# Performance work log

Hardware: AMD Instinct MI355X
Metric: run time of the kernel (lower is better)

Reference implementation:

```python
import jax, jax.numpy as jnp
import numpy as np

B, T, E, NH = 2, 2048, 512, 8
HD = E // NH
SCALE = float(HD) ** -0.5


def setup_inputs() -> dict:
    key = jax.random.key(0)
    ks = jax.random.split(key, 7)
    s = 0.02
    return {
        "x": jax.random.normal(ks[0], (B, T, E), dtype=jnp.float32),
        "w_qkv": jax.random.normal(ks[1], (E, 3 * E), dtype=jnp.float32) * s,
        "b_qkv": jax.random.normal(ks[2], (3 * E,), dtype=jnp.float32) * s,
        "w_od": jax.random.normal(ks[3], (E, 2 * NH), dtype=jnp.float32) * s,
        "b_od": jax.random.normal(ks[4], (2 * NH,), dtype=jnp.float32) * s,
        "w_out": jax.random.normal(ks[5], (E, E), dtype=jnp.float32) * s,
        "b_out": jax.random.normal(ks[6], (E,), dtype=jnp.float32) * s,
    }


def _heads(t):  # (B,T,E) -> (B*NH, T, HD)
    return t.reshape(B, T, NH, HD).transpose(0, 2, 1, 3).reshape(B * NH, T, HD)


def _point_mask(idx, j):  # idx: (B*NH,T) float indices -> one-hot (B*NH,T,T)
    return (j[None, None, :] == idx[:, :, None]).astype(jnp.float32)


def reference(x, w_qkv, b_qkv, w_od, b_od, w_out, b_out):
    qkv = x @ w_qkv + b_qkv
    Q, K, V = jnp.split(qkv, 3, axis=-1)  # each (B,T,E)

    od = Q @ w_od + b_od  # (B,T,2*NH)
    offset, duration = jnp.split(od, 2, axis=-1)
    offset = jnp.tanh(offset) * T
    duration = jax.nn.sigmoid(duration) * T

    query_index = jnp.arange(T, dtype=x.dtype)[None, :, None]  # (1,T,1)
    anchor = query_index + offset  # (B,T,NH)
    # 'b t nh -> (b nh) t'
    anchor = anchor.transpose(0, 2, 1).reshape(B * NH, T)
    duration = duration.transpose(0, 2, 1).reshape(B * NH, T)

    start = anchor - duration
    end = anchor + duration
    bound_l = jnp.floor(start)
    bound_r = jnp.ceil(end)
    anchor_l = jnp.floor(anchor)
    anchor_r = anchor_l + 1.0

    j = jnp.arange(T, dtype=x.dtype)
    neg_bound_weight = (bound_l - start)[:, :, None] * _point_mask(bound_l, j) \
                     + (end - bound_r)[:, :, None] * _point_mask(bound_r, j)
    anchor_dist_l = anchor - anchor_l
    anchor_weight = anchor_dist_l[:, :, None] * _point_mask(anchor_r, j) \
                  + (1.0 - anchor_dist_l)[:, :, None] * _point_mask(anchor_l, j)
    point_weight = 1.0 + neg_bound_weight + anchor_weight  # (B*NH,T,T)

    # segment mask: True OUTSIDE [bound_l, bound_r]
    attn_mask = (j[None, None, :] < bound_l[:, :, None]) | (j[None, None, :] > bound_r[:, :, None])

    Qh, Kh, Vh = _heads(Q), _heads(K), _heads(V)  # (B*NH, T, HD)
    scores = jnp.einsum('bic,brc->bir', Qh, Kh) * SCALE * point_weight
    scores = jnp.where(attn_mask, jnp.asarray(-1e8, scores.dtype), scores)
    attn = jax.nn.softmax(scores, axis=-1)
    out = jnp.einsum('bir,brc->bic', attn, Vh)  # (B*NH,T,HD)
    out = out.reshape(B, NH, T, HD).transpose(0, 2, 1, 3).reshape(B, T, E)
    return out @ w_out + b_out
```

## Files before the change

### kernel.cpp

```cpp
#include <hip/hip_runtime.h>
#include <math.h>

typedef float vf4 __attribute__((ext_vector_type(4)));
typedef float f32x4 __attribute__((ext_vector_type(4)));
typedef short bf16x8 __attribute__((ext_vector_type(8)));
typedef short short4v __attribute__((ext_vector_type(4)));

constexpr int B = 2, T = 2048, E = 512, NH = 8, HD = 64;
constexpr int BH = B * NH;
constexpr int NT = BH * T;
constexpr float SCALE = 0.125f;

static __device__ __forceinline__ short f2bf(float f) {
  unsigned u = __float_as_uint(f);
  unsigned r = (u + 0x7fffu + ((u >> 16) & 1u)) >> 16;
  return (short)r;
}

__global__ __launch_bounds__(256) void cast_x_bf16(
    const float* __restrict__ x, short* __restrict__ xb)
{
  int idx = (blockIdx.x * 256 + threadIdx.x) * 4;
  vf4 v = *(const vf4*)&x[idx];
  short4v o;
  o[0] = f2bf(v[0]); o[1] = f2bf(v[1]); o[2] = f2bf(v[2]); o[3] = f2bf(v[3]);
  *(short4v*)&xb[idx] = o;
}

__global__ __launch_bounds__(256) void cast_w_T(
    const float* __restrict__ w, short* __restrict__ wT, int N)
{
  __shared__ float t[32][33];
  const int k0 = blockIdx.x * 32;
  const int n0 = blockIdx.y * 32;
  const int c = threadIdx.x & 31, r = threadIdx.x >> 5;
#pragma unroll
  for (int p = 0; p < 4; ++p)
    t[r + p * 8][c] = w[(size_t)(k0 + r + p * 8) * N + n0 + c];
  __syncthreads();
#pragma unroll
  for (int p = 0; p < 4; ++p)
    wT[(size_t)(n0 + r + p * 8) * 512 + k0 + c] = f2bf(t[c][r + p * 8]);
}

__global__ __launch_bounds__(256) void w_comb(
    const float* __restrict__ w_qkv, const float* __restrict__ b_qkv,
    const float* __restrict__ w_od, const float* __restrict__ b_od,
    float* __restrict__ Wc, float* __restrict__ bc)
{
  const int tid = threadIdx.x;
  if (blockIdx.x < 32) {
    const int k = blockIdx.x * 16 + (tid >> 4);
    const int c = tid & 15;
    float s = 0.0f;
    for (int m = 0; m < E; ++m)
      s += w_qkv[(size_t)k * 1536 + m] * w_od[m * 16 + c];
    Wc[k * 16 + c] = s;
  } else if (tid < 16) {
    const int c = tid;
    float s = b_od[c];
    for (int m = 0; m < E; ++m)
      s += b_qkv[m] * w_od[m * 16 + c];
    bc[c] = s;
  }
}

__global__ __launch_bounds__(256) void qkv_gemm_bf16(
    const short* __restrict__ xb, const short* __restrict__ wT,
    const float* __restrict__ bias, short* __restrict__ qkvb)
{
  __shared__ short As[128 * 40];
  __shared__ short Bt[64 * 40];

  const int tid = threadIdx.x;
  const int wave = tid >> 6, lane = tid & 63;
  const int quad = lane >> 4, l15 = lane & 15;
  const int wm = wave >> 1, wn = wave & 1;
  const int m0 = blockIdx.y * 128, n0 = blockIdx.x * 64;

  f32x4 acc[4][2];
#pragma unroll
  for (int mi = 0; mi < 4; ++mi)
#pragma unroll
    for (int ni = 0; ni < 2; ++ni) acc[mi][ni] = (f32x4){0, 0, 0, 0};

  const int ar = tid >> 2, akc = (tid & 3) * 8;
  const int br_ = tid >> 2, bkc = (tid & 3) * 8;

#pragma unroll 1
  for (int k0 = 0; k0 < E; k0 += 32) {
    __syncthreads();
    *(bf16x8*)&As[ar * 40 + akc] =
        *(const bf16x8*)&xb[(size_t)(m0 + ar) * 512 + k0 + akc];
    *(bf16x8*)&As[(64 + ar) * 40 + akc] =
        *(const bf16x8*)&xb[(size_t)(m0 + 64 + ar) * 512 + k0 + akc];
    if (br_ < 64)
      *(bf16x8*)&Bt[br_ * 40 + bkc] =
          *(const bf16x8*)&wT[(size_t)(n0 + br_) * 512 + k0 + bkc];
    __syncthreads();

    bf16x8 aA[4], bB[2];
#pragma unroll
    for (int mi = 0; mi < 4; ++mi)
      aA[mi] = *(const bf16x8*)&As[(wm * 64 + mi * 16 + l15) * 40 + quad * 8];
#pragma unroll
    for (int ni = 0; ni < 2; ++ni)
      bB[ni] = *(const bf16x8*)&Bt[(wn * 32 + ni * 16 + l15) * 40 + quad * 8];
#pragma unroll
    for (int mi = 0; mi < 4; ++mi)
#pragma unroll
      for (int ni = 0; ni < 2; ++ni)
        acc[mi][ni] = __builtin_amdgcn_mfma_f32_16x16x32_bf16(
            aA[mi], bB[ni], acc[mi][ni], 0, 0, 0);
  }

#pragma unroll
  for (int mi = 0; mi < 4; ++mi)
#pragma unroll
    for (int ni = 0; ni < 2; ++ni)
#pragma unroll
      for (int r = 0; r < 4; ++r) {
        int row = m0 + wm * 64 + mi * 16 + quad * 4 + r;
        int col = n0 + wn * 32 + ni * 16 + l15;
        float v = acc[mi][ni][r] + bias[col];
        if (col < 512) v *= SCALE;
        qkvb[(size_t)row * 1536 + col] = f2bf(v);
      }
}

__global__ __launch_bounds__(256) void od_params(
    const float* __restrict__ x, const float* __restrict__ Wc,
    const float* __restrict__ bc, float* __restrict__ prm)
{
  __shared__ float od_s[16][16];
  const int tid = threadIdx.x;
  const int r = tid >> 4, c = tid & 15;
  const int row = blockIdx.x * 16 + r;

  float sum = bc[c];
  const float* qr = x + (size_t)row * E;
  for (int k = 0; k < E; k += 4) {
    vf4 q = *(const vf4*)&qr[k];
    sum += q[0] * Wc[(k + 0) * 16 + c]
         + q[1] * Wc[(k + 1) * 16 + c]
         + q[2] * Wc[(k + 2) * 16 + c]
         + q[3] * Wc[(k + 3) * 16 + c];
  }
  od_s[r][c] = sum;
  __syncthreads();

  if (tid < 128) {
    const int rr = tid >> 3, h = tid & 7;
    const int grow = blockIdx.x * 16 + rr;
    const int b = grow / T, i = grow % T;
    float o = od_s[rr][h];
    float d = od_s[rr][h + 8];
    float offset   = tanhf(o) * (float)T;
    float duration = (float)T / (1.0f + expf(-d));
    float anchor = (float)i + offset;
    float start = anchor - duration;
    float end   = anchor + duration;
    float bl = floorf(start);
    float br = ceilf(end);
    float al = floorf(anchor);
    float wbl = bl - start;
    float wbr = end - br;
    float af  = anchor - al;
    float rsc = 1.0f;
    if (br < 0.0f || bl > (float)(T - 1)) {
      bl = 0.0f; br = (float)(T - 1);
      wbl = 0.0f; wbr = 0.0f; al = -5.0f; af = 0.0f;
      rsc = 0.0f;
    }
    int idx = (b * NH + h) * T + i;
    prm[0 * NT + idx] = bl;
    prm[1 * NT + idx] = br;
    prm[2 * NT + idx] = wbl;
    prm[3 * NT + idx] = wbr;
    prm[4 * NT + idx] = al;
    prm[5 * NT + idx] = af;
    prm[6 * NT + idx] = rsc;
  }
}

__global__ __launch_bounds__(256) void flash_attn_mfma2(
    const short* __restrict__ qkvb, const float* __restrict__ prm,
    float* __restrict__ Opart, float* __restrict__ lpart)
{
  __shared__ short Qs[64 * 72];
  __shared__ short Ks[64 * 72];
  __shared__ short Vt[64 * 72];
  __shared__ short Ps[4][16 * 72];
  __shared__ float u_s[8];

  const int tid = threadIdx.x;
  const int wave = tid >> 6, lane = tid & 63;
  const int quad = lane >> 4, l15 = lane & 15;
  const int qt = blockIdx.x, bh = blockIdx.y, ks = blockIdx.z;
  const int b = bh >> 3, h = bh & 7;
  const int i0 = qt * 64;

  float bl[4], br[4], wbl[4], wbr[4], al[4], af[4], rsc[4];
  {
    int rowp = bh * T + i0 + wave * 16 + quad * 4;
#pragma unroll
    for (int r = 0; r < 4; ++r) {
      bl[r]  = prm[0 * NT + rowp + r];
      br[r]  = prm[1 * NT + rowp + r];
      wbl[r] = prm[2 * NT + rowp + r];
      wbr[r] = prm[3 * NT + rowp + r];
      al[r]  = prm[4 * NT + rowp + r];
      af[r]  = prm[5 * NT + rowp + r];
      rsc[r] = prm[6 * NT + rowp + r];
    }
  }

  float bmn = fminf(fminf(bl[0], bl[1]), fminf(bl[2], bl[3]));
  float bmx = fmaxf(fmaxf(br[0], br[1]), fmaxf(br[2], br[3]));
#pragma unroll
  for (int d = 16; d < 64; d <<= 1) {
    bmn = fminf(bmn, __shfl_xor(bmn, d));
    bmx = fmaxf(bmx, __shfl_xor(bmx, d));
  }
  if (lane == 0) { u_s[wave * 2] = bmn; u_s[wave * 2 + 1] = bmx; }

  {
    const int rq = tid >> 3, cb = (tid & 7) * 8;
#pragma unroll
    for (int it = 0; it < 2; ++it) {
      int rr = it * 32 + rq;
      *(bf16x8*)&Qs[rr * 72 + cb] =
          *(const bf16x8*)&qkvb[(size_t)(b * T + i0 + rr) * 1536 + h * 64 + cb];
    }
  }
  __syncthreads();
  bmn = fminf(fminf(u_s[0], u_s[2]), fminf(u_s[4], u_s[6]));
  bmx = fmaxf(fmaxf(u_s[1], u_s[3]), fmaxf(u_s[5], u_s[7]));
  const int ktlo = max(ks * 16, max(((int)bmn) >> 6, 0));
  const int kthi = min(ks * 16 + 15, min(((int)bmx) >> 6, T / 64 - 1));

  f32x4 o[4];
#pragma unroll
  for (int c = 0; c < 4; ++c) o[c] = (f32x4){0, 0, 0, 0};
  float lacc[4] = {0, 0, 0, 0};

  const int rq = tid >> 3, cb = (tid & 7) * 8;
  const int kw_sw = (cb >> 3) << 3;

#pragma unroll 1
  for (int kt = ktlo; kt <= kthi; ++kt) {
    const int j0 = kt * 64;
    __syncthreads();
#pragma unroll
    for (int it = 0; it < 2; ++it) {
      int rr = it * 32 + rq;
      size_t base = (size_t)(b * T + j0 + rr) * 1536 + h * 64 + cb;
      *(bf16x8*)&Ks[rr * 72 + cb] = *(const bf16x8*)&qkvb[base + 512];
      bf16x8 v = *(const bf16x8*)&qkvb[base + 1024];
      int kw = rr ^ kw_sw;
#pragma unroll
      for (int j = 0; j < 8; ++j) Vt[(cb + j) * 72 + kw] = v[j];
    }
    __syncthreads();

    bf16x8 aQ0 = *(const bf16x8*)&Qs[(wave * 16 + l15) * 72 + quad * 8];
    bf16x8 aQ1 = *(const bf16x8*)&Qs[(wave * 16 + l15) * 72 + 32 + quad * 8];
    f32x4 s[4];
#pragma unroll
    for (int nc = 0; nc < 4; ++nc) {
      const short* kb = &Ks[(nc * 16 + l15) * 72 + quad * 8];
      f32x4 a = (f32x4){0, 0, 0, 0};
      a = __builtin_amdgcn_mfma_f32_16x16x32_bf16(aQ0, *(const bf16x8*)&kb[0],  a, 0, 0, 0);
      a = __builtin_amdgcn_mfma_f32_16x16x32_bf16(aQ1, *(const bf16x8*)&kb[32], a, 0, 0, 0);
      s[nc] = a;
    }

    const float jf0 = (float)(j0 + l15);
#pragma unroll
    for (int nc = 0; nc < 4; ++nc) {
      float jf = jf0 + (float)(nc * 16);
#pragma unroll
      for (int r = 0; r < 4; ++r) {
        float w = 1.0f;
        w += (jf == bl[r]) ? wbl[r] : 0.0f;
        w += (jf == br[r]) ? wbr[r] : 0.0f;
        w += (jf == al[r]) ? (1.0f - af[r]) : 0.0f;
        w += (jf == al[r] + 1.0f) ? af[r] : 0.0f;
        float v = s[nc][r] * w * rsc[r];
        v = (jf < bl[r] || jf > br[r]) ? -30.0f : v;
        float p = __expf(v);
        lacc[r] += p;
        Ps[wave][(quad * 4 + r) * 72 + nc * 16 + l15] = f2bf(p);
      }
    }
    __syncthreads();

    bf16x8 aP0 = *(const bf16x8*)&Ps[wave][l15 * 72 + quad * 8];
    bf16x8 aP1 = *(const bf16x8*)&Ps[wave][l15 * 72 + 32 + quad * 8];
#pragma unroll
    for (int c = 0; c < 4; ++c) {
      int hd = c * 16 + l15;
      int g = (hd >> 3) & 7;
      const short* vb = &Vt[hd * 72];
      int blk0 = (quad) ^ g;
      int blk1 = (4 + quad) ^ g;
      o[c] = __builtin_amdgcn_mfma_f32_16x16x32_bf16(
          aP0, *(const bf16x8*)&vb[blk0 * 8], o[c], 0, 0, 0);
      o[c] = __builtin_amdgcn_mfma_f32_16x16x32_bf16(
          aP1, *(const bf16x8*)&vb[blk1 * 8], o[c], 0, 0, 0);
    }
  }

#pragma unroll
  for (int d = 1; d < 16; d <<= 1)
#pragma unroll
    for (int r = 0; r < 4; ++r)
      lacc[r] += __shfl_xor(lacc[r], d);

  const int rowb = i0 + wave * 16 + quad * 4;
  if (l15 == 0) {
#pragma unroll
    for (int r = 0; r < 4; ++r)
      lpart[ks * NT + bh * T + rowb + r] = lacc[r];
  }
#pragma unroll
  for (int r = 0; r < 4; ++r) {
    size_t base = (size_t)ks * (B * T * E) + (size_t)(b * T + rowb + r) * E + h * 64;
#pragma unroll
    for (int c = 0; c < 4; ++c)
      Opart[base + c * 16 + l15] = o[c][r];
  }
}

__global__ __launch_bounds__(256) void combine_attn(
    const float* __restrict__ Opart, const float* __restrict__ lpart,
    short* __restrict__ attnb)
{
  int base = (blockIdx.x * 256 + threadIdx.x) * 4;
  int row = base >> 9;
  int c = base & 511;
  int h = c >> 6;
  int b = row >> 11;
  int i = row & (T - 1);
  int lidx = ((b << 3) + h) * T + i;
  float l = lpart[lidx] + lpart[NT + lidx];
  float inv = 1.0f / l;
  vf4 o0 = *(const vf4*)&Opart[base];
  vf4 o1 = *(const vf4*)&Opart[(size_t)(B * T * E) + base];
  short4v ov;
#pragma unroll
  for (int j = 0; j < 4; ++j) ov[j] = f2bf((o0[j] + o1[j]) * inv);
  *(short4v*)&attnb[base] = ov;
}

__global__ __launch_bounds__(256) void out_gemm_bf16(
    const short* __restrict__ Ab, const short* __restrict__ wT,
    const float* __restrict__ bias, float* __restrict__ Co)
{
  __shared__ short As[64 * 40];
  __shared__ short Bt[64 * 40];

  const int tid = threadIdx.x;
  const int wave = tid >> 6, lane = tid & 63;
  const int quad = lane >> 4, l15 = lane & 15;
  const int wm = wave >> 1, wn = wave & 1;
  const int m0 = blockIdx.y * 64, n0 = blockIdx.x * 64;

  f32x4 acc[2][2];
#pragma unroll
  for (int mi = 0; mi < 2; ++mi)
#pragma unroll
    for (int ni = 0; ni < 2; ++ni) acc[mi][ni] = (f32x4){0, 0, 0, 0};

  const int ar = tid >> 2, akc = (tid & 3) * 8;

#pragma unroll 1
  for (int k0 = 0; k0 < E; k0 += 32) {
    __syncthreads();
    *(bf16x8*)&As[ar * 40 + akc] =
        *(const bf16x8*)&Ab[(size_t)(m0 + ar) * 512 + k0 + akc];
    *(bf16x8*)&Bt[ar * 40 + akc] =
        *(const bf16x8*)&wT[(size_t)(n0 + ar) * 512 + k0 + akc];
    __syncthreads();

    bf16x8 aA[2], bB[2];
#pragma unroll
    for (int mi = 0; mi < 2; ++mi)
      aA[mi] = *(const bf16x8*)&As[(wm * 32 + mi * 16 + l15) * 40 + quad * 8];
#pragma unroll
    for (int ni = 0; ni < 2; ++ni)
      bB[ni] = *(const bf16x8*)&Bt[(wn * 32 + ni * 16 + l15) * 40 + quad * 8];
#pragma unroll
    for (int mi = 0; mi < 2; ++mi)
#pragma unroll
      for (int ni = 0; ni < 2; ++ni)
        acc[mi][ni] = __builtin_amdgcn_mfma_f32_16x16x32_bf16(
            aA[mi], bB[ni], acc[mi][ni], 0, 0, 0);
  }

#pragma unroll
  for (int mi = 0; mi < 2; ++mi)
#pragma unroll
    for (int ni = 0; ni < 2; ++ni)
#pragma unroll
      for (int r = 0; r < 4; ++r) {
        int row = m0 + wm * 32 + mi * 16 + quad * 4 + r;
        int col = n0 + wn * 32 + ni * 16 + l15;
        Co[(size_t)row * 512 + col] = acc[mi][ni][r] + bias[col];
      }
}

extern "C" void kernel_launch(void* const* d_in, const int* in_sizes, int n_in,
                              void* d_out, int out_size, void* d_ws, size_t ws_size,
                              hipStream_t stream)
{
  const float* x     = (const float*)d_in[0];
  const float* w_qkv = (const float*)d_in[1];
  const float* b_qkv = (const float*)d_in[2];
  const float* w_od  = (const float*)d_in[3];
  const float* b_od  = (const float*)d_in[4];
  const float* w_out = (const float*)d_in[5];
  const float* b_out = (const float*)d_in[6];
  float* out = (float*)d_out;

  char* w = (char*)d_ws;
  short* xb    = (short*)w;  w += (size_t)B * T * E * 2;
  short* wTq   = (short*)w;  w += (size_t)E * 3 * E * 2;
  short* wTo   = (short*)w;  w += (size_t)E * E * 2;
  short* qkvb  = (short*)w;  w += (size_t)B * T * 3 * E * 2;
  float* Wc    = (float*)w;  w += (size_t)E * 16 * 4;
  float* bc    = (float*)w;  w += 256;
  float* prm   = (float*)w;  w += (size_t)7 * NT * 4;
  float* Opart = (float*)w;  w += (size_t)2 * B * T * E * 4;
  float* lpart = (float*)w;  w += (size_t)2 * NT * 4;
  short* attnb = (short*)w;  w += (size_t)B * T * E * 2;

  cast_x_bf16<<<dim3(B * T * E / 1024), 256, 0, stream>>>(x, xb);
  cast_w_T<<<dim3(E / 32, 3 * E / 32), 256, 0, stream>>>(w_qkv, wTq, 3 * E);
  cast_w_T<<<dim3(E / 32, E / 32), 256, 0, stream>>>(w_out, wTo, E);
  w_comb<<<dim3(33), 256, 0, stream>>>(w_qkv, b_qkv, w_od, b_od, Wc, bc);

  qkv_gemm_bf16<<<dim3(3 * E / 64, B * T / 128), 256, 0, stream>>>(
      xb, wTq, b_qkv, qkvb);

  od_params<<<dim3(B * T / 16), 256, 0, stream>>>(x, Wc, bc, prm);

  flash_attn_mfma2<<<dim3(T / 64, BH, 2), 256, 0, stream>>>(
      qkvb, prm, Opart, lpart);

  combine_attn<<<dim3(B * T * E / 1024), 256, 0, stream>>>(Opart, lpart, attnb);

  out_gemm_bf16<<<dim3(E / 64, B * T / 64), 256, 0, stream>>>(
      attnb, wTo, b_out, out);
}
```

Measured before the change: 197.3 us.

## Pretranspose V globally, swap MFMA operands in attention, widen QKV GEMM tile

Adds a separate kernel that transposes V into a head-major layout so the attention loop loads V tiles directly instead of scattering a transpose into shared memory every iteration. The attention kernel keeps Q in registers, swaps the MFMA operand order so each lane owns one query row, and replaces float comparisons for the point and segment weights with integer offset tests. It also writes P with packed stores, drops one barrier, and uses vectorised output stores. Separately, the QKV GEMM tile widens to 128x128, and w_comb stages w_od in shared memory and parallelises the bias reduction. The cost is an extra launch and one pass over V, with the transposed V reusing the xb buffer.

```diff
diff --git a/kernel.cpp b/kernel.cpp
--- a/kernel.cpp
+++ b/kernel.cpp
@@ -5,6 +5,7 @@
 typedef float f32x4 __attribute__((ext_vector_type(4)));
 typedef short bf16x8 __attribute__((ext_vector_type(8)));
 typedef short short4v __attribute__((ext_vector_type(4)));
+typedef int int2v __attribute__((ext_vector_type(2)));
 
 constexpr int B = 2, T = 2048, E = 512, NH = 8, HD = 64;
 constexpr int BH = B * NH;
@@ -15,6 +16,11 @@
   unsigned u = __float_as_uint(f);
   unsigned r = (u + 0x7fffu + ((u >> 16) & 1u)) >> 16;
   return (short)r;
+}
+static __device__ __forceinline__ unsigned pk2bf(float a, float b) {
+  unsigned lo = (unsigned)(unsigned short)f2bf(a);
+  unsigned hi = (unsigned)(unsigned short)f2bf(b);
+  return lo | (hi << 16);
 }
 
 __global__ __launch_bounds__(256) void cast_x_bf16(
@@ -48,20 +54,39 @@
     const float* __restrict__ w_od, const float* __restrict__ b_od,
     float* __restrict__ Wc, float* __restrict__ bc)
 {
-  const int tid = threadIdx.x;
+  __shared__ float Lod[512 * 16];
+  __shared__ float pb[16][17];
+  const int tid = threadIdx.x;
+#pragma unroll
+  for (int p = 0; p < 8; ++p) {
+    int idx = (p * 256 + tid) * 4;
+    *(vf4*)&Lod[idx] = *(const vf4*)&w_od[idx];
+  }
+  __syncthreads();
+
   if (blockIdx.x < 32) {
     const int k = blockIdx.x * 16 + (tid >> 4);
     const int c = tid & 15;
     float s = 0.0f;
-    for (int m = 0; m < E; ++m)
-      s += w_qkv[(size_t)k * 1536 + m] * w_od[m * 16 + c];
+    for (int m = 0; m < E; m += 4) {
+      vf4 wq = *(const vf4*)&w_qkv[(size_t)k * 1536 + m];
+      s += wq[0] * Lod[(m + 0) * 16 + c] + wq[1] * Lod[(m + 1) * 16 + c]
+         + wq[2] * Lod[(m + 2) * 16 + c] + wq[3] * Lod[(m + 3) * 16 + c];
+    }
     Wc[k * 16 + c] = s;
-  } else if (tid < 16) {
-    const int c = tid;
-    float s = b_od[c];
-    for (int m = 0; m < E; ++m)
-      s += b_qkv[m] * w_od[m * 16 + c];
-    bc[c] = s;
+  } else {
+    const int c = tid & 15, seg = tid >> 4;
+    float s = 0.0f;
+    for (int m = seg * 32; m < seg * 32 + 32; ++m)
+      s += b_qkv[m] * Lod[m * 16 + c];
+    pb[seg][c] = s;
+    __syncthreads();
+    if (tid < 16) {
+      float acc = b_od[tid];
+#pragma unroll
+      for (int g = 0; g < 16; ++g) acc += pb[g][tid];
+      bc[tid] = acc;
+    }
   }
 }
 
@@ -69,47 +94,47 @@
     const short* __restrict__ xb, const short* __restrict__ wT,
     const float* __restrict__ bias, short* __restrict__ qkvb)
 {
-  __shared__ short As[128 * 40];
-  __shared__ short Bt[64 * 40];
+  __shared__ __align__(16) short As[128 * 40];
+  __shared__ __align__(16) short Bt[128 * 40];
 
   const int tid = threadIdx.x;
   const int wave = tid >> 6, lane = tid & 63;
   const int quad = lane >> 4, l15 = lane & 15;
   const int wm = wave >> 1, wn = wave & 1;
-  const int m0 = blockIdx.y * 128, n0 = blockIdx.x * 64;
-
-  f32x4 acc[4][2];
+  const int m0 = blockIdx.y * 128, n0 = blockIdx.x * 128;
+
+  f32x4 acc[4][4];
 #pragma unroll
   for (int mi = 0; mi < 4; ++mi)
 #pragma unroll
-    for (int ni = 0; ni < 2; ++ni) acc[mi][ni] = (f32x4){0, 0, 0, 0};
-
-  const int ar = tid >> 2, akc = (tid & 3) * 8;
-  const int br_ = tid >> 2, bkc = (tid & 3) * 8;
+    for (int ni = 0; ni < 4; ++ni) acc[mi][ni] = (f32x4){0, 0, 0, 0};
+
+  const int sr = tid >> 1, sc = (tid & 1) * 16;
 
 #pragma unroll 1
   for (int k0 = 0; k0 < E; k0 += 32) {
     __syncthreads();
-    *(bf16x8*)&As[ar * 40 + akc] =
-        *(const bf16x8*)&xb[(size_t)(m0 + ar) * 512 + k0 + akc];
-    *(bf16x8*)&As[(64 + ar) * 40 + akc] =
-        *(const bf16x8*)&xb[(size_t)(m0 + 64 + ar) * 512 + k0 + akc];
-    if (br_ < 64)
-      *(bf16x8*)&Bt[br_ * 40 + bkc] =
-          *(const bf16x8*)&wT[(size_t)(n0 + br_) * 512 + k0 + bkc];
-    __syncthreads();
-
-    bf16x8 aA[4], bB[2];
+    *(bf16x8*)&As[sr * 40 + sc] =
+        *(const bf16x8*)&xb[(size_t)(m0 + sr) * 512 + k0 + sc];
+    *(bf16x8*)&As[sr * 40 + sc + 8] =
+        *(const bf16x8*)&xb[(size_t)(m0 + sr) * 512 + k0 + sc + 8];
+    *(bf16x8*)&Bt[sr * 40 + sc] =
+        *(const bf16x8*)&wT[(size_t)(n0 + sr) * 512 + k0 + sc];
+    *(bf16x8*)&Bt[sr * 40 + sc + 8] =
+        *(const bf16x8*)&wT[(size_t)(n0 + sr) * 512 + k0 + sc + 8];
+    __syncthreads();
+
+    bf16x8 aA[4], bB[4];
 #pragma unroll
     for (int mi = 0; mi < 4; ++mi)
       aA[mi] = *(const bf16x8*)&As[(wm * 64 + mi * 16 + l15) * 40 + quad * 8];
 #pragma unroll
-    for (int ni = 0; ni < 2; ++ni)
-      bB[ni] = *(const bf16x8*)&Bt[(wn * 32 + ni * 16 + l15) * 40 + quad * 8];
+    for (int ni = 0; ni < 4; ++ni)
+      bB[ni] = *(const bf16x8*)&Bt[(wn * 64 + ni * 16 + l15) * 40 + quad * 8];
 #pragma unroll
     for (int mi = 0; mi < 4; ++mi)
 #pragma unroll
-      for (int ni = 0; ni < 2; ++ni)
+      for (int ni = 0; ni < 4; ++ni)
         acc[mi][ni] = __builtin_amdgcn_mfma_f32_16x16x32_bf16(
             aA[mi], bB[ni], acc[mi][ni], 0, 0, 0);
   }
@@ -117,11 +142,11 @@
 #pragma unroll
   for (int mi = 0; mi < 4; ++mi)
 #pragma unroll
-    for (int ni = 0; ni < 2; ++ni)
+    for (int ni = 0; ni < 4; ++ni)
 #pragma unroll
       for (int r = 0; r < 4; ++r) {
         int row = m0 + wm * 64 + mi * 16 + quad * 4 + r;
-        int col = n0 + wn * 32 + ni * 16 + l15;
+        int col = n0 + wn * 64 + ni * 16 + l15;
         float v = acc[mi][ni][r] + bias[col];
         if (col < 512) v *= SCALE;
         qkvb[(size_t)row * 1536 + col] = f2bf(v);
@@ -183,14 +208,37 @@
   }
 }
 
-__global__ __launch_bounds__(256) void flash_attn_mfma2(
-    const short* __restrict__ qkvb, const float* __restrict__ prm,
+__global__ __launch_bounds__(256) void v_transpose(
+    const short* __restrict__ qkvb, short* __restrict__ Vtg)
+{
+  __shared__ __align__(16) short Tt[64 * 72];
+  const int tid = threadIdx.x;
+  const int t0 = blockIdx.x * 64, bh = blockIdx.y;
+  const int b = bh >> 3, h = bh & 7;
+  const int rq = tid >> 3, cb = (tid & 7) * 8;
+#pragma unroll
+  for (int it = 0; it < 2; ++it) {
+    int rr = it * 32 + rq;
+    bf16x8 v = *(const bf16x8*)&qkvb[(size_t)(b * T + t0 + rr) * 1536 + 1024 + h * 64 + cb];
+#pragma unroll
+    for (int j = 0; j < 8; ++j) Tt[(cb + j) * 72 + rr] = v[j];
+  }
+  __syncthreads();
+  const int hd = tid >> 2, tc = (tid & 3) * 16;
+  *(bf16x8*)&Vtg[(size_t)(bh * 64 + hd) * T + t0 + tc] =
+      *(const bf16x8*)&Tt[hd * 72 + tc];
+  *(bf16x8*)&Vtg[(size_t)(bh * 64 + hd) * T + t0 + tc + 8] =
+      *(const bf16x8*)&Tt[hd * 72 + tc + 8];
+}
+
+__global__ __launch_bounds__(256, 4) void flash_attn_mfma3(
+    const short* __restrict__ qkvb, const short* __restrict__ Vtg,
+    const float* __restrict__ prm,
     float* __restrict__ Opart, float* __restrict__ lpart)
 {
-  __shared__ short Qs[64 * 72];
-  __shared__ short Ks[64 * 72];
-  __shared__ short Vt[64 * 72];
-  __shared__ short Ps[4][16 * 72];
+  __shared__ __align__(16) short Ks[64 * 72];
+  __shared__ __align__(16) short Vt[64 * 72];
+  __shared__ __align__(16) short Ps[4][16 * 72];
   __shared__ float u_s[8];
 
   const int tid = threadIdx.x;
@@ -199,40 +247,38 @@
   const int qt = blockIdx.x, bh = blockIdx.y, ks = blockIdx.z;
   const int b = bh >> 3, h = bh & 7;
   const int i0 = qt * 64;
-
-  float bl[4], br[4], wbl[4], wbr[4], al[4], af[4], rsc[4];
+  const int i = i0 + wave * 16 + l15;
+
+  const int pidx = bh * T + i;
+  float blf = prm[0 * NT + pidx];
+  float brf = prm[1 * NT + pidx];
+  float wbl = prm[2 * NT + pidx];
+  float wbr = prm[3 * NT + pidx];
+  float alf = prm[4 * NT + pidx];
+  float afr = prm[5 * NT + pidx];
+  float rsc = prm[6 * NT + pidx];
+  const int bli = (int)blf, widi = (int)brf - bli, ali = (int)alf;
+  const unsigned widu = (unsigned)widi;
+  const float a1 = 1.0f - afr;
+
+  bf16x8 aQ0, aQ1;
   {
-    int rowp = bh * T + i0 + wave * 16 + quad * 4;
-#pragma unroll
-    for (int r = 0; r < 4; ++r) {
-      bl[r]  = prm[0 * NT + rowp + r];
-      br[r]  = prm[1 * NT + rowp + r];
-      wbl[r] = prm[2 * NT + rowp + r];
-      wbr[r] = prm[3 * NT + rowp + r];
-      al[r]  = prm[4 * NT + rowp + r];
-      af[r]  = prm[5 * NT + rowp + r];
-      rsc[r] = prm[6 * NT + rowp + r];
-    }
-  }
-
-  float bmn = fminf(fminf(bl[0], bl[1]), fminf(bl[2], bl[3]));
-  float bmx = fmaxf(fmaxf(br[0], br[1]), fmaxf(br[2], br[3]));
-#pragma unroll
-  for (int d = 16; d < 64; d <<= 1) {
+    size_t bq = (size_t)(b * T + i) * 1536 + h * 64;
+    aQ0 = *(const bf16x8*)&qkvb[bq + quad * 8];
+    aQ1 = *(const bf16x8*)&qkvb[bq + 32 + quad * 8];
+    if (rsc == 0.0f) {
+      bf16x8 z = {0, 0, 0, 0, 0, 0, 0, 0};
+      aQ0 = z; aQ1 = z;
+    }
+  }
+
+  float bmn = blf, bmx = brf;
+#pragma unroll
+  for (int d = 1; d < 64; d <<= 1) {
     bmn = fminf(bmn, __shfl_xor(bmn, d));
     bmx = fmaxf(bmx, __shfl_xor(bmx, d));
   }
   if (lane == 0) { u_s[wave * 2] = bmn; u_s[wave * 2 + 1] = bmx; }
-
-  {
-    const int rq = tid >> 3, cb = (tid & 7) * 8;
-#pragma unroll
-    for (int it = 0; it < 2; ++it) {
-      int rr = it * 32 + rq;
-      *(bf16x8*)&Qs[rr * 72 + cb] =
-          *(const bf16x8*)&qkvb[(size_t)(b * T + i0 + rr) * 1536 + h * 64 + cb];
-    }
-  }
   __syncthreads();
   bmn = fminf(fminf(u_s[0], u_s[2]), fminf(u_s[4], u_s[6]));
   bmx = fmaxf(fmaxf(u_s[1], u_s[3]), fmaxf(u_s[5], u_s[7]));
@@ -242,10 +288,9 @@
   f32x4 o[4];
 #pragma unroll
   for (int c = 0; c < 4; ++c) o[c] = (f32x4){0, 0, 0, 0};
-  float lacc[4] = {0, 0, 0, 0};
+  float lacc = 0.0f;
 
   const int rq = tid >> 3, cb = (tid & 7) * 8;
-  const int kw_sw = (cb >> 3) << 3;
 
 #pragma unroll 1
   for (int kt = ktlo; kt <= kthi; ++kt) {
@@ -254,82 +299,68 @@
 #pragma unroll
     for (int it = 0; it < 2; ++it) {
       int rr = it * 32 + rq;
-      size_t base = (size_t)(b * T + j0 + rr) * 1536 + h * 64 + cb;
-      *(bf16x8*)&Ks[rr * 72 + cb] = *(const bf16x8*)&qkvb[base + 512];
-      bf16x8 v = *(const bf16x8*)&qkvb[base + 1024];
-      int kw = rr ^ kw_sw;
-#pragma unroll
-      for (int j = 0; j < 8; ++j) Vt[(cb + j) * 72 + kw] = v[j];
-    }
-    __syncthreads();
-
-    bf16x8 aQ0 = *(const bf16x8*)&Qs[(wave * 16 + l15) * 72 + quad * 8];
-    bf16x8 aQ1 = *(const bf16x8*)&Qs[(wave * 16 + l15) * 72 + 32 + quad * 8];
+      *(bf16x8*)&Ks[rr * 72 + cb] =
+          *(const bf16x8*)&qkvb[(size_t)(b * T + j0 + rr) * 1536 + 512 + h * 64 + cb];
+      *(bf16x8*)&Vt[rr * 72 + cb] =
+          *(const bf16x8*)&Vtg[(size_t)(bh * 64 + rr) * T + j0 + cb];
+    }
+    __syncthreads();
+
     f32x4 s[4];
 #pragma unroll
     for (int nc = 0; nc < 4; ++nc) {
       const short* kb = &Ks[(nc * 16 + l15) * 72 + quad * 8];
       f32x4 a = (f32x4){0, 0, 0, 0};
-      a = __builtin_amdgcn_mfma_f32_16x16x32_bf16(aQ0, *(const bf16x8*)&kb[0],  a, 0, 0, 0);
-      a = __builtin_amdgcn_mfma_f32_16x16x32_bf16(aQ1, *(const bf16x8*)&kb[32], a, 0, 0, 0);
+      a = __builtin_amdgcn_mfma_f32_16x16x32_bf16(*(const bf16x8*)&kb[0],  aQ0, a, 0, 0, 0);
+      a = __builtin_amdgcn_mfma_f32_16x16x32_bf16(*(const bf16x8*)&kb[32], aQ1, a, 0, 0, 0);
       s[nc] = a;
     }
 
-    const float jf0 = (float)(j0 + l15);
+    const int dq  = j0 + quad * 4 - bli;
+    const int dq2 = j0 + quad * 4 - ali;
 #pragma unroll
     for (int nc = 0; nc < 4; ++nc) {
-      float jf = jf0 + (float)(nc * 16);
+      const int dn = dq + nc * 16, d2n = dq2 + nc * 16;
+      float pr[4];
 #pragma unroll
       for (int r = 0; r < 4; ++r) {
-        float w = 1.0f;
-        w += (jf == bl[r]) ? wbl[r] : 0.0f;
-        w += (jf == br[r]) ? wbr[r] : 0.0f;
-        w += (jf == al[r]) ? (1.0f - af[r]) : 0.0f;
-        w += (jf == al[r] + 1.0f) ? af[r] : 0.0f;
-        float v = s[nc][r] * w * rsc[r];
-        v = (jf < bl[r] || jf > br[r]) ? -30.0f : v;
+        int d = dn + r, d2 = d2n + r;
+        float e  = (d == 0) ? wbl : ((d == widi) ? wbr : 0.0f);
+        float aw = (d2 == 0) ? a1 : ((d2 == 1) ? afr : 0.0f);
+        float w = 1.0f + e + aw;
+        float v = s[nc][r] * w;
+        v = ((unsigned)d <= widu) ? v : -80.0f;
         float p = __expf(v);
-        lacc[r] += p;
-        Ps[wave][(quad * 4 + r) * 72 + nc * 16 + l15] = f2bf(p);
+        lacc += p;
+        pr[r] = p;
       }
-    }
-    __syncthreads();
-
-    bf16x8 aP0 = *(const bf16x8*)&Ps[wave][l15 * 72 + quad * 8];
-    bf16x8 aP1 = *(const bf16x8*)&Ps[wave][l15 * 72 + 32 + quad * 8];
-#pragma unroll
-    for (int c = 0; c < 4; ++c) {
-      int hd = c * 16 + l15;
-      int g = (hd >> 3) & 7;
-      const short* vb = &Vt[hd * 72];
-      int blk0 = (quad) ^ g;
-      int blk1 = (4 + quad) ^ g;
-      o[c] = __builtin_amdgcn_mfma_f32_16x16x32_bf16(
-          aP0, *(const bf16x8*)&vb[blk0 * 8], o[c], 0, 0, 0);
-      o[c] = __builtin_amdgcn_mfma_f32_16x16x32_bf16(
-          aP1, *(const bf16x8*)&vb[blk1 * 8], o[c], 0, 0, 0);
-    }
-  }
-
-#pragma unroll
-  for (int d = 1; d < 16; d <<= 1)
-#pragma unroll
-    for (int r = 0; r < 4; ++r)
-      lacc[r] += __shfl_xor(lacc[r], d);
-
-  const int rowb = i0 + wave * 16 + quad * 4;
-  if (l15 == 0) {
-#pragma unroll
-    for (int r = 0; r < 4; ++r)
-      lpart[ks * NT + bh * T + rowb + r] = lacc[r];
-  }
-#pragma unroll
-  for (int r = 0; r < 4; ++r) {
-    size_t base = (size_t)ks * (B * T * E) + (size_t)(b * T + rowb + r) * E + h * 64;
-#pragma unroll
-    for (int c = 0; c < 4; ++c)
-      Opart[base + c * 16 + l15] = o[c][r];
-  }
+      int2v pk;
+      pk[0] = (int)pk2bf(pr[0], pr[1]);
+      pk[1] = (int)pk2bf(pr[2], pr[3]);
+      *(int2v*)&Ps[wave][l15 * 72 + nc * 16 + quad * 4] = pk;
+    }
+
+    bf16x8 bP0 = *(const bf16x8*)&Ps[wave][l15 * 72 + quad * 8];
+    bf16x8 bP1 = *(const bf16x8*)&Ps[wave][l15 * 72 + 32 + quad * 8];
+#pragma unroll
+    for (int nc2 = 0; nc2 < 4; ++nc2) {
+      const short* vb = &Vt[(nc2 * 16 + l15) * 72 + quad * 8];
+      o[nc2] = __builtin_amdgcn_mfma_f32_16x16x32_bf16(
+          *(const bf16x8*)&vb[0],  bP0, o[nc2], 0, 0, 0);
+      o[nc2] = __builtin_amdgcn_mfma_f32_16x16x32_bf16(
+          *(const bf16x8*)&vb[32], bP1, o[nc2], 0, 0, 0);
+    }
+  }
+
+  lacc += __shfl_xor(lacc, 16);
+  lacc += __shfl_xor(lacc, 32);
+  if (lane < 16)
+    lpart[ks * NT + bh * T + i] = lacc;
+
+  size_t ob = (size_t)ks * (B * T * E) + (size_t)(b * T + i) * E + h * 64;
+#pragma unroll
+  for (int nc2 = 0; nc2 < 4; ++nc2)
+    *(f32x4*)&Opart[ob + nc2 * 16 + quad * 4] = o[nc2];
 }
 
 __global__ __launch_bounds__(256) void combine_attn(
@@ -357,8 +388,8 @@
     const short* __restrict__ Ab, const short* __restrict__ wT,
     const float* __restrict__ bias, float* __restrict__ Co)
 {
-  __shared__ short As[64 * 40];
-  __shared__ short Bt[64 * 40];
+  __shared__ __align__(16) short As[64 * 40];
+  __shared__ __align__(16) short Bt[64 * 40];
 
   const int tid = threadIdx.x;
   const int wave = tid >> 6, lane = tid & 63;
@@ -434,19 +465,22 @@
   float* Opart = (float*)w;  w += (size_t)2 * B * T * E * 4;
   float* lpart = (float*)w;  w += (size_t)2 * NT * 4;
   short* attnb = (short*)w;  w += (size_t)B * T * E * 2;
+  short* Vtg   = xb;
 
   cast_x_bf16<<<dim3(B * T * E / 1024), 256, 0, stream>>>(x, xb);
   cast_w_T<<<dim3(E / 32, 3 * E / 32), 256, 0, stream>>>(w_qkv, wTq, 3 * E);
   cast_w_T<<<dim3(E / 32, E / 32), 256, 0, stream>>>(w_out, wTo, E);
   w_comb<<<dim3(33), 256, 0, stream>>>(w_qkv, b_qkv, w_od, b_od, Wc, bc);
 
-  qkv_gemm_bf16<<<dim3(3 * E / 64, B * T / 128), 256, 0, stream>>>(
+  qkv_gemm_bf16<<<dim3(3 * E / 128, B * T / 128), 256, 0, stream>>>(
       xb, wTq, b_qkv, qkvb);
 
   od_params<<<dim3(B * T / 16), 256, 0, stream>>>(x, Wc, bc, prm);
 
-  flash_attn_mfma2<<<dim3(T / 64, BH, 2), 256, 0, stream>>>(
-      qkvb, prm, Opart, lpart);
+  v_transpose<<<dim3(T / 64, BH), 256, 0, stream>>>(qkvb, Vtg);
+
+  flash_attn_mfma3<<<dim3(T / 64, BH, 2), 256, 0, stream>>>(
+      qkvb, Vtg, prm, Opart, lpart);
 
   combine_attn<<<dim3(B * T * E / 1024), 256, 0, stream>>>(Opart, lpart, attnb);
 
```

After: 197.8 us. Within noise of the previous version (+0.3%).
